# Kernel optimization log

Hardware: AMD Instinct MI355X
Metric: run time of the kernel (lower is better)

## Reference

```python
import jax, jax.numpy as jnp
import numpy as np

E = 16          # n_routed_experts
Z = 8           # zero_expert_num
K = 4           # moe_topk
H = 1024        # hidden_size
I = 768         # moe_intermediate_size
T = 2048        # tokens
SCALE = 2.5     # routed_scaling_factor


def setup_inputs() -> dict:
    key = jax.random.key(0)
    ks = jax.random.split(key, 6)
    return {
        "hidden_states": jax.random.normal(ks[0], (T, H), dtype=jnp.float32),
        "num_global_tokens": T,
        "max_num_tokens_per_gpu": T,
        "w_router": jax.random.normal(ks[1], (E + Z, H), dtype=jnp.float32) * 0.02,
        "correction_bias": jnp.zeros((E + Z,), dtype=jnp.float32),
        "wg": jax.random.normal(ks[2], (E, I, H), dtype=jnp.float32) * 0.02,
        "wu": jax.random.normal(ks[3], (E, I, H), dtype=jnp.float32) * 0.02,
        "wd": jax.random.normal(ks[4], (E, H, I), dtype=jnp.float32) * 0.02,
    }


def reference(hidden_states, num_global_tokens, max_num_tokens_per_gpu,
              w_router, correction_bias, wg, wu, wd):
    x = hidden_states
    # ---- router gemm (always fp32) ----
    logits = x.astype(jnp.float32) @ w_router.T                      # [T, E+Z]
    # ---- DeepSeekV3-style top-k: sigmoid scores, bias only for selection ----
    scores = jax.nn.sigmoid(logits)
    _, topk_ids = jax.lax.top_k(scores + correction_bias[None, :], K)  # [T, K]
    w = jnp.take_along_axis(scores, topk_ids, axis=-1)               # [T, K]
    w = w / jnp.sum(w, axis=-1, keepdims=True)                       # renormalize
    w = w * SCALE                                                    # routed_scaling_factor
    # ---- zero-expert masking (identity type) ----
    zero_mask = topk_ids >= E                                        # [T, K]
    zero_w = jnp.sum(jnp.where(zero_mask, w, 0.0), axis=-1, keepdims=True)
    ids = jnp.where(zero_mask, 0, topk_ids)
    w = jnp.where(zero_mask, 0.0, w)
    # ---- combine weights per (token, expert); masked slots add 0.0 ----
    cw = jnp.zeros((x.shape[0], E), dtype=jnp.float32)
    cw = cw.at[jnp.arange(x.shape[0])[:, None], ids].add(w)          # [T, E]
    # ---- grouped silu-gated expert MLPs (dense compute + masked combine) ----
    g = jnp.einsum('th,eih->eti', x, wg)                             # [E, T, I]
    u = jnp.einsum('th,eih->eti', x, wu)
    a = jax.nn.silu(g) * u
    y = jnp.einsum('eti,ehi->eth', a, wd)                            # [E, T, H]
    routed = jnp.einsum('eth,te->th', y, cw)                         # [T, H]
    return routed + x * zero_w.astype(x.dtype)
```

## Files before the change

### kernel.cpp

```cpp
#include <hip/hip_runtime.h>
#include <hip/hip_bf16.h>
#include <math.h>

typedef __bf16 bf16x8 __attribute__((ext_vector_type(8)));
typedef float f32x4 __attribute__((ext_vector_type(4)));

#define T_TOK 2048
#define HD 1024
#define ID 768
#define NE 16
#define NEZ 24
#define NK 4
#define SCALE_F 2.5f

#define MFMA(a, b, c) __builtin_amdgcn_mfma_f32_16x16x32_bf16(a, b, c, 0, 0, 0)

__device__ __forceinline__ unsigned short f2bf(float f) {
  unsigned int u = __builtin_bit_cast(unsigned int, f);
  u += 0x7FFFu + ((u >> 16) & 1u);
  return (unsigned short)(u >> 16);
}

__device__ __forceinline__ bf16x8 cvt8(float4 a, float4 b) {
  bf16x8 t;
  t[0] = (__bf16)a.x; t[1] = (__bf16)a.y; t[2] = (__bf16)a.z; t[3] = (__bf16)a.w;
  t[4] = (__bf16)b.x; t[5] = (__bf16)b.y; t[6] = (__bf16)b.z; t[7] = (__bf16)b.w;
  return t;
}

__device__ __forceinline__ void gload16(const void* g, void* l) {
  __builtin_amdgcn_global_load_lds(
      (const __attribute__((address_space(1))) void*)(unsigned long long)(uintptr_t)g,
      (__attribute__((address_space(3))) void*)(uintptr_t)l, 16, 0, 0);
}

__global__ __launch_bounds__(256) void router_k(
    const float* __restrict__ x, const float* __restrict__ wr,
    const float* __restrict__ bias,
    int* __restrict__ counts, int* __restrict__ lists, float* __restrict__ wlist,
    unsigned short* __restrict__ xb, float* __restrict__ out) {
  const int wave = threadIdx.x >> 6, l = threadIdx.x & 63;
  const int t = blockIdx.x * 4 + wave;

  float4 xr[4];
#pragma unroll
  for (int c = 0; c < 4; ++c)
    xr[c] = *(const float4*)(x + (size_t)t * HD + c * 256 + l * 4);
#pragma unroll
  for (int c = 0; c < 4; ++c) {
    ushort4 h;
    h.x = f2bf(xr[c].x); h.y = f2bf(xr[c].y); h.z = f2bf(xr[c].z); h.w = f2bf(xr[c].w);
    *(ushort4*)(xb + (size_t)t * HD + c * 256 + l * 4) = h;
  }

  float acc[NEZ];
#pragma unroll 4
  for (int e = 0; e < NEZ; ++e) {
    float4 s = {0.f, 0.f, 0.f, 0.f};
#pragma unroll
    for (int c = 0; c < 4; ++c) {
      float4 w4 = *(const float4*)(wr + (size_t)e * HD + c * 256 + l * 4);
      s.x = fmaf(w4.x, xr[c].x, s.x); s.y = fmaf(w4.y, xr[c].y, s.y);
      s.z = fmaf(w4.z, xr[c].z, s.z); s.w = fmaf(w4.w, xr[c].w, s.w);
    }
    acc[e] = (s.x + s.y) + (s.z + s.w);
  }
#pragma unroll
  for (int s = 1; s < 64; s <<= 1) {
#pragma unroll
    for (int e = 0; e < NEZ; ++e) acc[e] += __shfl_xor(acc[e], s);
  }
  float sc[NEZ], scb[NEZ];
#pragma unroll
  for (int e = 0; e < NEZ; ++e) {
    float s = 1.f / (1.f + expf(-acc[e]));
    sc[e] = s;
    scb[e] = s + bias[e];
  }
  unsigned picked = 0;
  int ids[NK]; float wv[NK]; float ssum = 0.f;
#pragma unroll
  for (int k = 0; k < NK; ++k) {
    int best = 0; float bv = -1e30f; float bsc = 0.f;
#pragma unroll
    for (int e = 0; e < NEZ; ++e) {
      bool take = (((picked >> e) & 1u) == 0) && (scb[e] > bv);
      best = take ? e : best;
      bv = take ? scb[e] : bv;
      bsc = take ? sc[e] : bsc;
    }
    picked |= 1u << best;
    ids[k] = best; wv[k] = bsc; ssum += bsc;
  }
  const float inv = SCALE_F / ssum;
  float zw = 0.f;
#pragma unroll
  for (int k = 0; k < NK; ++k)
    zw += (ids[k] >= NE) ? wv[k] * inv : 0.f;
  if (l < NK) {
    int id = ids[l];
    if (id < NE) {
      int p = atomicAdd(&counts[id], 1);
      lists[id * T_TOK + p] = t;
      wlist[id * T_TOK + p] = wv[l] * inv;
    }
  }
#pragma unroll
  for (int c = 0; c < 4; ++c) {
    float4 o;
    o.x = xr[c].x * zw; o.y = xr[c].y * zw;
    o.z = xr[c].z * zw; o.w = xr[c].w * zw;
    *(float4*)(out + (size_t)t * HD + c * 256 + l * 4) = o;
  }
}

__global__ __launch_bounds__(256, 3) void gu_k(
    const unsigned short* __restrict__ xb,
    const float* __restrict__ wg, const float* __restrict__ wu,
    const float* __restrict__ wd, unsigned short* __restrict__ wdb,
    const int* __restrict__ counts,
    const int* __restrict__ lists, unsigned short* __restrict__ abuf) {
  const int b = blockIdx.x;
  if (b >= 3072) {
    const size_t base = (size_t)(b - 3072) * 24576 + threadIdx.x * 4;
#pragma unroll
    for (int i = 0; i < 24; ++i) {
      float4 v = *(const float4*)(wd + base + (size_t)i * 1024);
      ushort4 h;
      h.x = f2bf(v.x); h.y = f2bf(v.y); h.z = f2bf(v.z); h.w = f2bf(v.w);
      *(ushort4*)(wdb + base + (size_t)i * 1024) = h;
    }
    return;
  }
  const int L = (b & 7) * 384 + (b >> 3);
  const int e = L / 192;
  const int rem = L % 192;
  const int xs = rem / 16, ys = rem % 16;
  const int cnt = counts[e];
  const int m0 = ys * 128;
  if (m0 >= cnt) return;
  const int n0 = xs * 64;

  int offs_e = 0;
  for (int i = 0; i < e; ++i) offs_e += counts[i];

  __shared__ int toks[128];
  __shared__ char lds[2][24576];

  const int tid = threadIdx.x;
  if (tid < 128) {
    int m = m0 + tid;
    toks[tid] = (m < cnt) ? lists[e * T_TOK + m] : 0;
  }
  __syncthreads();

  const unsigned short* asrc[2];
#pragma unroll
  for (int j = 0; j < 2; ++j) {
    int row = j * 64 + (tid >> 2);
    int c = ((tid & 3) - (row >> 1)) & 3;
    asrc[j] = xb + (size_t)toks[row] * HD + c * 8;
  }
  const size_t wbase = (size_t)e * ID * HD;
  const float* gsrc[2]; const float* usrc[2];
#pragma unroll
  for (int j = 0; j < 2; ++j) {
    int row = j * 32 + (tid >> 3);
    int c = ((tid & 7) - row) & 7;
    size_t ro = wbase + (size_t)(n0 + row) * HD + c * 4;
    gsrc[j] = wg + ro; usrc[j] = wu + ro;
  }

  const int wid = tid >> 6, l = tid & 63;
  const int wm = (wid >> 1) * 64, wn = (wid & 1) * 32;
  const int q = l >> 4, r = l & 15;

  f32x4 ag[4][2] = {}; f32x4 au[4][2] = {};

  auto stage = [&](int bb, int k0) {
    char* dst = &lds[bb][0] + tid * 16;
#pragma unroll
    for (int j = 0; j < 2; ++j) {
      gload16(asrc[j] + k0, dst + j * 4096);
      gload16(gsrc[j] + k0, dst + 8192 + j * 4096);
      gload16(usrc[j] + k0, dst + 16384 + j * 4096);
    }
  };
  auto comp = [&](int bb) {
    const char* base = &lds[bb][0];
    bf16x8 a[4];
#pragma unroll
    for (int fm = 0; fm < 4; ++fm) {
      int rr = wm + fm * 16 + r;
      int p = (q + (rr >> 1)) & 3;
      a[fm] = *(const bf16x8*)(base + rr * 64 + p * 16);
    }
#pragma unroll
    for (int fn = 0; fn < 2; ++fn) {
      int cc = wn + fn * 16 + r;
      int p0 = (2 * q + cc) & 7, p1 = (2 * q + 1 + cc) & 7;
      const char* pg = base + 8192 + cc * 128;
      const char* pu = base + 16384 + cc * 128;
      float4 g0 = *(const float4*)(pg + p0 * 16);
      float4 g1 = *(const float4*)(pg + p1 * 16);
      float4 u0 = *(const float4*)(pu + p0 * 16);
      float4 u1 = *(const float4*)(pu + p1 * 16);
      bf16x8 bg = cvt8(g0, g1), bu = cvt8(u0, u1);
#pragma unroll
      for (int fm = 0; fm < 4; ++fm) {
        ag[fm][fn] = MFMA(a[fm], bg, ag[fm][fn]);
        au[fm][fn] = MFMA(a[fm], bu, au[fm][fn]);
      }
    }
  };

  stage(0, 0);
  __syncthreads();
  for (int t = 0; t < 32; t += 2) {
    stage(1, (t + 1) * 32);
    comp(0);
    __syncthreads();
    if (t + 2 < 32) stage(0, (t + 2) * 32);
    comp(1);
    __syncthreads();
  }

  const int rowbase = offs_e + m0;
#pragma unroll
  for (int fm = 0; fm < 4; ++fm)
#pragma unroll
    for (int fn = 0; fn < 2; ++fn)
#pragma unroll
      for (int i2 = 0; i2 < 4; ++i2) {
        int mr = wm + fm * 16 + q * 4 + i2;
        if (m0 + mr < cnt) {
          float g = ag[fm][fn][i2], u = au[fm][fn][i2];
          float s = 1.0f / (1.0f + expf(-g));
          float aa = g * s * u;
          int col = n0 + wn + fn * 16 + r;
          abuf[(size_t)(rowbase + mr) * ID + col] = f2bf(aa);
        }
      }
}

__global__ __launch_bounds__(256, 3) void dn_k(
    const unsigned short* __restrict__ abuf,
    const unsigned short* __restrict__ wdb,
    const int* __restrict__ counts,
    const int* __restrict__ lists, const float* __restrict__ wlist,
    float* __restrict__ out) {
  const int b = blockIdx.x;
  const int L = (b & 7) * 512 + (b >> 3);
  const int e = L / 256;
  const int rem = L % 256;
  const int xs = rem / 16, ys = rem % 16;
  const int cnt = counts[e];
  const int m0 = ys * 128;
  if (m0 >= cnt) return;
  const int n0 = xs * 64;

  int offs_e = 0;
  for (int i = 0; i < e; ++i) offs_e += counts[i];

  __shared__ char lds[2][24576];

  const int tid = threadIdx.x;

  const unsigned short* asrc[4];
#pragma unroll
  for (int j = 0; j < 4; ++j) {
    int u = j * 256 + tid;
    int row = u >> 3;
    int c = ((u & 7) - row) & 7;
    int m = m0 + row; if (m >= cnt) m = cnt - 1;
    asrc[j] = abuf + (size_t)(offs_e + m) * ID + c * 8;
  }
  const unsigned short* bsrc[2];
#pragma unroll
  for (int j = 0; j < 2; ++j) {
    int u = j * 256 + tid;
    int row = u >> 3;
    int c = ((u & 7) - row) & 7;
    bsrc[j] = wdb + (size_t)e * HD * ID + (size_t)(n0 + row) * ID + c * 8;
  }

  const int wid = tid >> 6, l = tid & 63;
  const int wm = (wid >> 1) * 64, wn = (wid & 1) * 32;
  const int q = l >> 4, r = l & 15;

  f32x4 acc[4][2] = {};

  auto stage = [&](int bb, int k0) {
    char* dst = &lds[bb][0] + tid * 16;
#pragma unroll
    for (int j = 0; j < 4; ++j) gload16(asrc[j] + k0, dst + j * 4096);
#pragma unroll
    for (int j = 0; j < 2; ++j) gload16(bsrc[j] + k0, dst + 16384 + j * 4096);
  };
  auto comp = [&](int bb) {
    const char* base = &lds[bb][0];
#pragma unroll
    for (int kk = 0; kk < 2; ++kk) {
      bf16x8 a[4];
#pragma unroll
      for (int fm = 0; fm < 4; ++fm) {
        int rr = wm + fm * 16 + r;
        int kc = kk * 4 + q;
        a[fm] = *(const bf16x8*)(base + rr * 128 + (((kc + rr) & 7) << 4));
      }
#pragma unroll
      for (int fn = 0; fn < 2; ++fn) {
        int cc = wn + fn * 16 + r;
        int kc = kk * 4 + q;
        bf16x8 bb2 = *(const bf16x8*)(base + 16384 + cc * 128 + (((kc + cc) & 7) << 4));
#pragma unroll
        for (int fm = 0; fm < 4; ++fm)
          acc[fm][fn] = MFMA(a[fm], bb2, acc[fm][fn]);
      }
    }
  };

  stage(0, 0);
  __syncthreads();
  for (int t = 0; t < 12; t += 2) {
    stage(1, (t + 1) * 64);
    comp(0);
    __syncthreads();
    if (t + 2 < 12) stage(0, (t + 2) * 64);
    comp(1);
    __syncthreads();
  }

#pragma unroll
  for (int fm = 0; fm < 4; ++fm) {
#pragma unroll
    for (int i2 = 0; i2 < 4; ++i2) {
      int mr = wm + fm * 16 + q * 4 + i2;
      if (m0 + mr < cnt) {
        int tok = lists[e * T_TOK + m0 + mr];
        float wt = wlist[e * T_TOK + m0 + mr];
#pragma unroll
        for (int fn = 0; fn < 2; ++fn) {
          int col = n0 + wn + fn * 16 + r;
          atomicAdd(&out[(size_t)tok * HD + col], acc[fm][fn][i2] * wt);
        }
      }
    }
  }
}

extern "C" void kernel_launch(void* const* d_in, const int* in_sizes, int n_in,
                              void* d_out, int out_size, void* d_ws, size_t ws_size,
                              hipStream_t stream) {
  (void)in_sizes; (void)n_in; (void)out_size; (void)ws_size;
  const float* x    = (const float*)d_in[0];
  const float* wr   = (const float*)d_in[3];
  const float* bias = (const float*)d_in[4];
  const float* wg   = (const float*)d_in[5];
  const float* wu   = (const float*)d_in[6];
  const float* wd   = (const float*)d_in[7];
  float* out = (float*)d_out;

  char* p = (char*)d_ws;
  auto alloc = [&](size_t bytes) {
    char* r = p;
    p += (bytes + 255) & ~(size_t)255;
    return r;
  };
  int*   counts  = (int*)alloc(NE * 4);
  int*   lists   = (int*)alloc((size_t)NE * T_TOK * 4);
  float* wlist   = (float*)alloc((size_t)NE * T_TOK * 4);
  unsigned short* xb   = (unsigned short*)alloc((size_t)T_TOK * HD * 2);
  unsigned short* abuf = (unsigned short*)alloc((size_t)(T_TOK * NK + 128) * ID * 2);
  unsigned short* wdb  = (unsigned short*)alloc((size_t)NE * HD * ID * 2);

  hipMemsetAsync(counts, 0, NE * 4, stream);
  router_k<<<T_TOK / 4, 256, 0, stream>>>(x, wr, bias, counts, lists, wlist, xb, out);
  gu_k<<<3584, 256, 0, stream>>>(xb, wg, wu, wd, wdb, counts, lists, abuf);
  dn_k<<<4096, 256, 0, stream>>>(abuf, wdb, counts, lists, wlist, out);
}
```

Before: 131.8 us.

## Pre-convert gate/up weights to bf16 in router kernel and stream bf16 tiles

```diff
diff --git a/kernel.cpp b/kernel.cpp
--- a/kernel.cpp
+++ b/kernel.cpp
@@ -21,13 +21,6 @@
   return (unsigned short)(u >> 16);
 }
 
-__device__ __forceinline__ bf16x8 cvt8(float4 a, float4 b) {
-  bf16x8 t;
-  t[0] = (__bf16)a.x; t[1] = (__bf16)a.y; t[2] = (__bf16)a.z; t[3] = (__bf16)a.w;
-  t[4] = (__bf16)b.x; t[5] = (__bf16)b.y; t[6] = (__bf16)b.z; t[7] = (__bf16)b.w;
-  return t;
-}
-
 __device__ __forceinline__ void gload16(const void* g, void* l) {
   __builtin_amdgcn_global_load_lds(
       (const __attribute__((address_space(1))) void*)(unsigned long long)(uintptr_t)g,
@@ -37,8 +30,27 @@
 __global__ __launch_bounds__(256) void router_k(
     const float* __restrict__ x, const float* __restrict__ wr,
     const float* __restrict__ bias,
+    const float* __restrict__ wg, const float* __restrict__ wu,
+    const float* __restrict__ wd,
+    unsigned short* __restrict__ wgb, unsigned short* __restrict__ wub,
+    unsigned short* __restrict__ wdb,
     int* __restrict__ counts, int* __restrict__ lists, float* __restrict__ wlist,
     unsigned short* __restrict__ xb, float* __restrict__ out) {
+  if (blockIdx.x >= 512) {
+    const int ci = blockIdx.x - 512;
+    const int w = ci / 384, blk = ci % 384;
+    const float* src = (w == 0) ? wg : (w == 1) ? wu : wd;
+    unsigned short* dst = (w == 0) ? wgb : (w == 1) ? wub : wdb;
+    const size_t base = (size_t)blk * 32768 + threadIdx.x * 4;
+#pragma unroll
+    for (int i = 0; i < 32; ++i) {
+      float4 v = *(const float4*)(src + base + (size_t)i * 1024);
+      ushort4 h;
+      h.x = f2bf(v.x); h.y = f2bf(v.y); h.z = f2bf(v.z); h.w = f2bf(v.w);
+      *(ushort4*)(dst + base + (size_t)i * 1024) = h;
+    }
+    return;
+  }
   const int wave = threadIdx.x >> 6, l = threadIdx.x & 63;
   const int t = blockIdx.x * 4 + wave;
 
@@ -114,24 +126,12 @@
   }
 }
 
-__global__ __launch_bounds__(256, 3) void gu_k(
+__global__ __launch_bounds__(256, 4) void gu_k(
     const unsigned short* __restrict__ xb,
-    const float* __restrict__ wg, const float* __restrict__ wu,
-    const float* __restrict__ wd, unsigned short* __restrict__ wdb,
+    const unsigned short* __restrict__ wgb, const unsigned short* __restrict__ wub,
     const int* __restrict__ counts,
     const int* __restrict__ lists, unsigned short* __restrict__ abuf) {
   const int b = blockIdx.x;
-  if (b >= 3072) {
-    const size_t base = (size_t)(b - 3072) * 24576 + threadIdx.x * 4;
-#pragma unroll
-    for (int i = 0; i < 24; ++i) {
-      float4 v = *(const float4*)(wd + base + (size_t)i * 1024);
-      ushort4 h;
-      h.x = f2bf(v.x); h.y = f2bf(v.y); h.z = f2bf(v.z); h.w = f2bf(v.w);
-      *(ushort4*)(wdb + base + (size_t)i * 1024) = h;
-    }
-    return;
-  }
   const int L = (b & 7) * 384 + (b >> 3);
   const int e = L / 192;
   const int rem = L % 192;
@@ -145,7 +145,7 @@
   for (int i = 0; i < e; ++i) offs_e += counts[i];
 
   __shared__ int toks[128];
-  __shared__ char lds[2][24576];
+  __shared__ char lds[2][16384];
 
   const int tid = threadIdx.x;
   if (tid < 128) {
@@ -157,18 +157,18 @@
   const unsigned short* asrc[2];
 #pragma unroll
   for (int j = 0; j < 2; ++j) {
-    int row = j * 64 + (tid >> 2);
+    int u = j * 256 + tid;
+    int row = u >> 2;
+    int c = ((u & 3) - (row >> 1)) & 3;
+    asrc[j] = xb + (size_t)toks[row] * HD + c * 8;
+  }
+  const size_t wbase = (size_t)e * ID * HD;
+  const unsigned short* gsrc; const unsigned short* usrc;
+  {
+    int row = tid >> 2;
     int c = ((tid & 3) - (row >> 1)) & 3;
-    asrc[j] = xb + (size_t)toks[row] * HD + c * 8;
-  }
-  const size_t wbase = (size_t)e * ID * HD;
-  const float* gsrc[2]; const float* usrc[2];
-#pragma unroll
-  for (int j = 0; j < 2; ++j) {
-    int row = j * 32 + (tid >> 3);
-    int c = ((tid & 7) - row) & 7;
-    size_t ro = wbase + (size_t)(n0 + row) * HD + c * 4;
-    gsrc[j] = wg + ro; usrc[j] = wu + ro;
+    size_t ro = wbase + (size_t)(n0 + row) * HD + c * 8;
+    gsrc = wgb + ro; usrc = wub + ro;
   }
 
   const int wid = tid >> 6, l = tid & 63;
@@ -178,13 +178,12 @@
   f32x4 ag[4][2] = {}; f32x4 au[4][2] = {};
 
   auto stage = [&](int bb, int k0) {
-    char* dst = &lds[bb][0] + tid * 16;
-#pragma unroll
-    for (int j = 0; j < 2; ++j) {
-      gload16(asrc[j] + k0, dst + j * 4096);
-      gload16(gsrc[j] + k0, dst + 8192 + j * 4096);
-      gload16(usrc[j] + k0, dst + 16384 + j * 4096);
-    }
+    char* base = &lds[bb][0];
+#pragma unroll
+    for (int j = 0; j < 2; ++j)
+      gload16(asrc[j] + k0, base + (j * 256 + tid) * 16);
+    gload16(gsrc + k0, base + 8192 + tid * 16);
+    gload16(usrc + k0, base + 12288 + tid * 16);
   };
   auto comp = [&](int bb) {
     const char* base = &lds[bb][0];
@@ -198,14 +197,9 @@
 #pragma unroll
     for (int fn = 0; fn < 2; ++fn) {
       int cc = wn + fn * 16 + r;
-      int p0 = (2 * q + cc) & 7, p1 = (2 * q + 1 + cc) & 7;
-      const char* pg = base + 8192 + cc * 128;
-      const char* pu = base + 16384 + cc * 128;
-      float4 g0 = *(const float4*)(pg + p0 * 16);
-      float4 g1 = *(const float4*)(pg + p1 * 16);
-      float4 u0 = *(const float4*)(pu + p0 * 16);
-      float4 u1 = *(const float4*)(pu + p1 * 16);
-      bf16x8 bg = cvt8(g0, g1), bu = cvt8(u0, u1);
+      int p = (q + (cc >> 1)) & 3;
+      bf16x8 bg = *(const bf16x8*)(base + 8192 + cc * 64 + p * 16);
+      bf16x8 bu = *(const bf16x8*)(base + 12288 + cc * 64 + p * 16);
 #pragma unroll
       for (int fm = 0; fm < 4; ++fm) {
         ag[fm][fn] = MFMA(a[fm], bg, ag[fm][fn]);
@@ -372,10 +366,13 @@
   float* wlist   = (float*)alloc((size_t)NE * T_TOK * 4);
   unsigned short* xb   = (unsigned short*)alloc((size_t)T_TOK * HD * 2);
   unsigned short* abuf = (unsigned short*)alloc((size_t)(T_TOK * NK + 128) * ID * 2);
+  unsigned short* wgb  = (unsigned short*)alloc((size_t)NE * ID * HD * 2);
+  unsigned short* wub  = (unsigned short*)alloc((size_t)NE * ID * HD * 2);
   unsigned short* wdb  = (unsigned short*)alloc((size_t)NE * HD * ID * 2);
 
   hipMemsetAsync(counts, 0, NE * 4, stream);
-  router_k<<<T_TOK / 4, 256, 0, stream>>>(x, wr, bias, counts, lists, wlist, xb, out);
-  gu_k<<<3584, 256, 0, stream>>>(xb, wg, wu, wd, wdb, counts, lists, abuf);
+  router_k<<<1664, 256, 0, stream>>>(x, wr, bias, wg, wu, wd, wgb, wub, wdb,
+                                     counts, lists, wlist, xb, out);
+  gu_k<<<3072, 256, 0, stream>>>(xb, wgb, wub, counts, lists, abuf);
   dn_k<<<4096, 256, 0, stream>>>(abuf, wdb, counts, lists, wlist, out);
 }
```

New measurement: 141.1 us. 7.0% more time.
